# Kernel optimization log

Hardware: AMD Instinct MI355X
Metric: run time of the kernel (lower is better)

Reference implementation:

```python
import jax, jax.numpy as jnp
import numpy as np

NHEAD, HEAD_DIM, UNFOLD = 16, 64, 3
SCALE = np.float32(1.0 / np.sqrt(HEAD_DIM))


def setup_inputs() -> dict:
    key = jax.random.key(0)
    ks = jax.random.split(key, 10)
    B, C, N, L, aL = 1, 256, 64, 256, 2
    D = NHEAD * HEAD_DIM  # 1024
    return {
        "x": jax.random.normal(ks[0], (B, C, N, L, 1), dtype=jnp.float32),
        "ax": jax.random.normal(ks[1], (B, C, N, aL, L), dtype=jnp.float32),
        "wq": jax.random.normal(ks[2], (D, C), dtype=jnp.float32) * 0.02,
        "bq": jax.random.normal(ks[3], (D,), dtype=jnp.float32) * 0.02,
        "wk": jax.random.normal(ks[4], (D, C), dtype=jnp.float32) * 0.02,
        "bk": jax.random.normal(ks[5], (D,), dtype=jnp.float32) * 0.02,
        "wv": jax.random.normal(ks[6], (D, C), dtype=jnp.float32) * 0.02,
        "bv": jax.random.normal(ks[7], (D,), dtype=jnp.float32) * 0.02,
        "wo": jax.random.normal(ks[8], (C, D), dtype=jnp.float32) * 0.02,
        "bo": jax.random.normal(ks[9], (C,), dtype=jnp.float32) * 0.02,
    }


def _proj(x, w, b):
    # x: [B,C,N,L], w: [D,C] -> [B,D,N,L]  (1x1x1 Conv3d == pointwise GEMM)
    return jnp.einsum('bcnl,dc->bdnl', x, w) + b[None, :, None, None]


def reference(x, ax, wq, bq, wk, bk, wv, bv, wo, bo):
    B, C, N, L, _ = x.shape
    x4 = x[..., 0]  # [B,C,N,L]
    q = _proj(x4, wq, bq).reshape(B, NHEAD, HEAD_DIM, N, 1, L)
    k4 = _proj(x4, wk, bk)
    v4 = _proj(x4, wv, bv)

    def unfold(t):
        # F.unfold kernel (3,1), padding (1,0) along N, then the original's
        # .view(B, nhead, head_dim, N, 3, L) applied to [B, C*3, N*L]
        tp = jnp.pad(t, ((0, 0), (0, 0), (1, 1), (0, 0)))
        tw = jnp.stack([tp[:, :, i:i + N, :] for i in range(UNFOLD)], axis=2)  # [B,D,3,N,L]
        return tw.reshape(B, NHEAD, HEAD_DIM, UNFOLD, N, L).reshape(
            B, NHEAD, HEAD_DIM, N, UNFOLD, L)

    k = unfold(k4)
    v = unfold(v4)

    aL = ax.shape[3]
    ak = (jnp.einsum('bcnal,dc->bdnal', ax, wk)
          + bk[None, :, None, None, None]).reshape(B, NHEAD, HEAD_DIM, N, aL, L)
    av = (jnp.einsum('bcnal,dc->bdnal', ax, wv)
          + bv[None, :, None, None, None]).reshape(B, NHEAD, HEAD_DIM, N, aL, L)
    k = jnp.concatenate([k, ak], axis=4)  # [B,H,d,N,3+aL,L]
    v = jnp.concatenate([v, av], axis=4)

    scores = (q * k).sum(2, keepdims=True) * SCALE        # [B,H,1,N,W,L]
    alphas = jax.nn.softmax(scores, axis=4)               # dropout=eval -> identity
    att = (alphas * v).sum(4).reshape(B, NHEAD * HEAD_DIM, N, L)
    out = jnp.einsum('bdnl,cd->bcnl', att, wo) + bo[None, :, None, None]
    return out[..., None]  # [B,nhid,N,L,1]
```

## Files before the change

kernel.cpp:

```cpp
#include <hip/hip_runtime.h>
#include <hip/hip_bf16.h>
#include <stdint.h>

#define N_HEAD 16
#define HDIM 64
#define C_IN 256
#define D_MODEL 1024
#define N_SP 64
#define L_SP 256
#define A_L 2
#define MS (N_SP * L_SP)
#define MA (N_SP * A_L * L_SP)
#define MT (MS + MA)
#define ATT_SCALE 0.125f
#define AUXP 136

typedef __attribute__((ext_vector_type(8))) short bf16x8;
typedef __attribute__((ext_vector_type(4))) float f32x4;
typedef __attribute__((ext_vector_type(8))) unsigned short u16x8;
typedef __attribute__((ext_vector_type(4))) unsigned int u32x4;

static __device__ __forceinline__ __hip_bfloat16 f2bf(float v) { return __float2bfloat16(v); }
static __device__ __forceinline__ unsigned short bfbits(float v) {
    union { __hip_bfloat16 h; unsigned short u; } cv;
    cv.h = __float2bfloat16(v);
    return cv.u;
}
static __device__ __forceinline__ float s2f(short u) {
    union { unsigned int i; float f; } c;
    c.i = ((unsigned int)(unsigned short)u) << 16;
    return c.f;
}

__global__ __launch_bounds__(256) void prep_weights(
    const float* __restrict__ wq, const float* __restrict__ bq,
    const float* __restrict__ wk, const float* __restrict__ bk,
    const float* __restrict__ wv, const float* __restrict__ bv,
    const float* __restrict__ wo,
    __hip_bfloat16* __restrict__ Wqkv, float* __restrict__ BiasQKV,
    __hip_bfloat16* __restrict__ WoB)
{
    int idx = blockIdx.x * 256 + threadIdx.x;
    int row = idx >> 8, col = idx & 255;
    const float* w = (row < D_MODEL) ? wq : (row < 2 * D_MODEL) ? wk : wv;
    Wqkv[idx] = f2bf(w[(size_t)(row & (D_MODEL - 1)) * C_IN + col]);
    if (col == 0) {
        const float* b = (row < D_MODEL) ? bq : (row < 2 * D_MODEL) ? bk : bv;
        BiasQKV[row] = b[row & (D_MODEL - 1)];
    }
    if (idx < C_IN * D_MODEL) WoB[idx] = f2bf(wo[idx]);
}

__global__ __launch_bounds__(256) void transpose_in(
    const float* __restrict__ x, const float* __restrict__ ax,
    __hip_bfloat16* __restrict__ XtAll)
{
    __shared__ float tile[32][33];
    const int tx = threadIdx.x, ty = threadIdx.y;
    const int bx = blockIdx.x;
    const float* src; int M, m0, drow0;
    if (bx < MS / 32) { src = x;  M = MS; m0 = bx * 32;              drow0 = m0; }
    else              { src = ax; M = MA; m0 = (bx - MS / 32) * 32;  drow0 = MS + m0; }
    const int c0 = blockIdx.y * 32;
#pragma unroll
    for (int j = 0; j < 32; j += 8)
        tile[ty + j][tx] = src[(size_t)(c0 + ty + j) * M + m0 + tx];
    __syncthreads();
#pragma unroll
    for (int j = 0; j < 32; j += 8)
        XtAll[(size_t)(drow0 + ty + j) * C_IN + c0 + tx] = f2bf(tile[tx][ty + j]);
}

__global__ __launch_bounds__(256) void gemm_proj(
    const __hip_bfloat16* __restrict__ A,
    const __hip_bfloat16* __restrict__ B,
    __hip_bfloat16* __restrict__ C,
    const float* __restrict__ bias,
    int M, int N, int K)
{
    __shared__ __align__(16) __hip_bfloat16 As[128 * 64];
    __shared__ __align__(16) __hip_bfloat16 Bs[128 * 64];

    const int tid = threadIdx.x;
    const int lane = tid & 63;
    const int w = tid >> 6;
    const int wr = w >> 1, wc = w & 1;
    const int fr = lane & 15, fq = lane >> 4;

    const int nwg = gridDim.x * gridDim.y;
    const int lin = blockIdx.y * gridDim.x + blockIdx.x;
    const int qq = nwg >> 3, rr = nwg & 7;
    const int xcd = lin & 7, ix = lin >> 3;
    const int nlin = (xcd < rr) ? xcd * (qq + 1) + ix
                                : rr * (qq + 1) + (xcd - rr) * qq + ix;
    const int bx = nlin % gridDim.x, by = nlin / gridDim.x;

    const int i0 = by * 128, j0 = bx * 128;
    const int srow = tid >> 3, sch = (tid & 7) << 3;

    f32x4 acc[4][4];
#pragma unroll
    for (int a = 0; a < 4; ++a)
#pragma unroll
        for (int b = 0; b < 4; ++b) acc[a][b] = (f32x4){0.f, 0.f, 0.f, 0.f};

    for (int k0 = 0; k0 < K; k0 += 64) {
        u32x4 ra[4], rb[4];
#pragma unroll
        for (int is = 0; is < 4; ++is) {
            int row = is * 32 + srow;
            ra[is] = *(const u32x4*)(A + (size_t)(i0 + row) * K + k0 + sch);
            rb[is] = *(const u32x4*)(B + (size_t)(j0 + row) * K + k0 + sch);
        }
#pragma unroll
        for (int is = 0; is < 4; ++is) {
            int row = is * 32 + srow;
            *(u32x4*)(As + row * 64 + sch) = ra[is];
            *(u32x4*)(Bs + row * 64 + sch) = rb[is];
        }
        __syncthreads();
#pragma unroll
        for (int kk = 0; kk < 64; kk += 32) {
            bf16x8 af[4], bb[4];
#pragma unroll
            for (int mi = 0; mi < 4; ++mi)
                af[mi] = *(const bf16x8*)(As + (wr * 64 + mi * 16 + fr) * 64 + kk + fq * 8);
#pragma unroll
            for (int ni = 0; ni < 4; ++ni)
                bb[ni] = *(const bf16x8*)(Bs + (wc * 64 + ni * 16 + fr) * 64 + kk + fq * 8);
#pragma unroll
            for (int mi = 0; mi < 4; ++mi)
#pragma unroll
                for (int ni = 0; ni < 4; ++ni)
                    acc[mi][ni] = __builtin_amdgcn_mfma_f32_16x16x32_bf16(
                        af[mi], bb[ni], acc[mi][ni], 0, 0, 0);
        }
        __syncthreads();
    }

#pragma unroll
    for (int mi = 0; mi < 4; ++mi)
#pragma unroll
        for (int r = 0; r < 4; ++r) {
            int row = i0 + wr * 64 + mi * 16 + fq * 4 + r;
#pragma unroll
            for (int ni = 0; ni < 4; ++ni) {
                int col = j0 + wc * 64 + ni * 16 + fr;
                C[(size_t)row * N + col] = f2bf(acc[mi][ni][r] + bias[col]);
            }
        }
}

__global__ __launch_bounds__(256) void attn_fused(
    const __hip_bfloat16* __restrict__ XtAll,
    const __hip_bfloat16* __restrict__ Wqkv,
    const float* __restrict__ BiasQKV,
    __hip_bfloat16* qkv)
{
    __shared__ __align__(16) char ldsraw[36864];
    __hip_bfloat16* As  = (__hip_bfloat16*)ldsraw;
    __hip_bfloat16* Bs  = (__hip_bfloat16*)(ldsraw + 16384);
    __hip_bfloat16* aux = (__hip_bfloat16*)ldsraw;

    const int flat = blockIdx.x;
    const int xcd = flat & 7, idx = flat >> 3;
    const int n  = xcd * 8 + (idx & 7);
    const int h  = (idx >> 3) & 15;
    const int lt = idx >> 7;

    const int tid = threadIdx.x;
    const int lane = tid & 63;
    const int w = tid >> 6;
    const int wr = w >> 1, wc = w & 1;
    const int fr = lane & 15, fq = lane >> 4;
    const int srow = tid >> 3, sch = (tid & 7) << 3;

    f32x4 acc[4][4];
#pragma unroll
    for (int a = 0; a < 4; ++a)
#pragma unroll
        for (int b = 0; b < 4; ++b) acc[a][b] = (f32x4){0.f, 0.f, 0.f, 0.f};

    for (int k0 = 0; k0 < 256; k0 += 64) {
        u32x4 ra[4], rb[4];
#pragma unroll
        for (int is = 0; is < 4; ++is) {
            int r = is * 32 + srow;
            int arow = MS + n * 512 + (r >> 6) * 256 + lt * 64 + (r & 63);
            int brow = 1024 + (r >> 6) * 1024 + h * 64 + (r & 63);
            ra[is] = *(const u32x4*)(XtAll + (size_t)arow * 256 + k0 + sch);
            rb[is] = *(const u32x4*)(Wqkv + (size_t)brow * 256 + k0 + sch);
        }
#pragma unroll
        for (int is = 0; is < 4; ++is) {
            int r = is * 32 + srow;
            *(u32x4*)(As + r * 64 + sch) = ra[is];
            *(u32x4*)(Bs + r * 64 + sch) = rb[is];
        }
        __syncthreads();
#pragma unroll
        for (int kk = 0; kk < 64; kk += 32) {
            bf16x8 af[4], bb[4];
#pragma unroll
            for (int mi = 0; mi < 4; ++mi)
                af[mi] = *(const bf16x8*)(As + (wr * 64 + mi * 16 + fr) * 64 + kk + fq * 8);
#pragma unroll
            for (int ni = 0; ni < 4; ++ni)
                bb[ni] = *(const bf16x8*)(Bs + (wc * 64 + ni * 16 + fr) * 64 + kk + fq * 8);
#pragma unroll
            for (int mi = 0; mi < 4; ++mi)
#pragma unroll
                for (int ni = 0; ni < 4; ++ni)
                    acc[mi][ni] = __builtin_amdgcn_mfma_f32_16x16x32_bf16(
                        af[mi], bb[ni], acc[mi][ni], 0, 0, 0);
        }
        __syncthreads();
    }

    float bcol[4];
#pragma unroll
    for (int ni = 0; ni < 4; ++ni)
        bcol[ni] = BiasQKV[1024 + wc * 1024 + h * 64 + ni * 16 + fr];

#pragma unroll
    for (int mi = 0; mi < 4; ++mi)
#pragma unroll
        for (int r = 0; r < 4; ++r) {
            int row = wr * 64 + mi * 16 + fq * 4 + r;
#pragma unroll
            for (int ni = 0; ni < 4; ++ni) {
                int col = wc * 64 + ni * 16 + fr;
                aux[row * AUXP + col] = f2bf(acc[mi][ni][r] + bcol[ni]);
            }
        }
    __syncthreads();

    const int sub = tid & 3;
    const int ll = tid >> 2;
    const int l = lt * 64 + ll;
    const int m = n * L_SP + l;
    const int ch = sub * 16;

    int src[3]; float val[3];
#pragma unroll
    for (int wd = 0; wd < 3; ++wd) {
        int f = n * 3 + wd;
        int un = f >> 6;
        int nn = (f & 63) + un - 1;
        bool ok = (nn >= 0) && (nn < N_SP);
        src[wd] = ok ? nn : 0;
        val[wd] = ok ? 1.f : 0.f;
    }

    __hip_bfloat16* qp = qkv + (size_t)m * 3072 + h * 64 + ch;
    bf16x8 q0 = *(const bf16x8*)qp, q1 = *(const bf16x8*)(qp + 8);

    bf16x8 kg[3][2], vg[3][2];
#pragma unroll
    for (int wd = 0; wd < 3; ++wd) {
        const __hip_bfloat16* rowp = qkv + (size_t)(src[wd] * L_SP + l) * 3072 + h * 64 + ch;
        kg[wd][0] = *(const bf16x8*)(rowp + 1024);
        kg[wd][1] = *(const bf16x8*)(rowp + 1024 + 8);
        vg[wd][0] = *(const bf16x8*)(rowp + 2048);
        vg[wd][1] = *(const bf16x8*)(rowp + 2048 + 8);
    }
    bf16x8 ka[2][2], va[2][2];
#pragma unroll
    for (int a = 0; a < 2; ++a) {
        const __hip_bfloat16* base = aux + (a * 64 + ll) * AUXP;
        ka[a][0] = *(const bf16x8*)(base + ch);
        ka[a][1] = *(const bf16x8*)(base + ch + 8);
        va[a][0] = *(const bf16x8*)(base + 64 + ch);
        va[a][1] = *(const bf16x8*)(base + 64 + ch + 8);
    }

    float s[5];
#pragma unroll
    for (int i = 0; i < 3; ++i) {
        float d = 0.f;
#pragma unroll
        for (int j = 0; j < 8; ++j)
            d += s2f(q0[j]) * s2f(kg[i][0][j]) + s2f(q1[j]) * s2f(kg[i][1][j]);
        s[i] = d;
    }
#pragma unroll
    for (int a = 0; a < 2; ++a) {
        float d = 0.f;
#pragma unroll
        for (int j = 0; j < 8; ++j)
            d += s2f(q0[j]) * s2f(ka[a][0][j]) + s2f(q1[j]) * s2f(ka[a][1][j]);
        s[3 + a] = d;
    }
#pragma unroll
    for (int i = 0; i < 5; ++i) {
        s[i] += __shfl_xor(s[i], 1);
        s[i] += __shfl_xor(s[i], 2);
        s[i] *= ATT_SCALE;
    }
    s[0] *= val[0]; s[1] *= val[1]; s[2] *= val[2];

    float mx = fmaxf(fmaxf(fmaxf(s[0], s[1]), fmaxf(s[2], s[3])), s[4]);
    float e0 = __expf(s[0] - mx), e1 = __expf(s[1] - mx), e2 = __expf(s[2] - mx);
    float e3 = __expf(s[3] - mx), e4 = __expf(s[4] - mx);
    float inv = 1.f / (e0 + e1 + e2 + e3 + e4);
    float al[5];
    al[0] = e0 * inv * val[0];
    al[1] = e1 * inv * val[1];
    al[2] = e2 * inv * val[2];
    al[3] = e3 * inv;
    al[4] = e4 * inv;

#pragma unroll
    for (int g = 0; g < 2; ++g) {
        u16x8 pack;
#pragma unroll
        for (int j = 0; j < 8; ++j) {
            float o = al[0] * s2f(vg[0][g][j]) + al[1] * s2f(vg[1][g][j])
                    + al[2] * s2f(vg[2][g][j]) + al[3] * s2f(va[0][g][j])
                    + al[4] * s2f(va[1][g][j]);
            pack[j] = bfbits(o);
        }
        *(u16x8*)(qp + g * 8) = pack;
    }
}

__global__ __launch_bounds__(256) void gemm_out(
    const __hip_bfloat16* __restrict__ A,
    const __hip_bfloat16* __restrict__ B,
    float* __restrict__ C,
    const float* __restrict__ bo)
{
    __shared__ __align__(16) __hip_bfloat16 As[128 * 64];
    __shared__ __align__(16) __hip_bfloat16 Bs[128 * 64];

    const int tid = threadIdx.x;
    const int lane = tid & 63;
    const int w = tid >> 6;
    const int wr = w >> 1, wc = w & 1;
    const int fr = lane & 15, fq = lane >> 4;

    const int nwg = gridDim.x * gridDim.y;
    const int lin = blockIdx.y * gridDim.x + blockIdx.x;
    const int qq = nwg >> 3, rr = nwg & 7;
    const int xcd = lin & 7, ix = lin >> 3;
    const int nlin = (xcd < rr) ? xcd * (qq + 1) + ix
                                : rr * (qq + 1) + (xcd - rr) * qq + ix;
    const int bx = nlin % gridDim.x, by = nlin / gridDim.x;

    const int i0 = by * 128, j0 = bx * 128;
    const int srow = tid >> 3, sch = (tid & 7) << 3;

    f32x4 acc[4][4];
#pragma unroll
    for (int a = 0; a < 4; ++a)
#pragma unroll
        for (int b = 0; b < 4; ++b) acc[a][b] = (f32x4){0.f, 0.f, 0.f, 0.f};

    for (int k0 = 0; k0 < 1024; k0 += 64) {
        u32x4 ra[4], rb[4];
#pragma unroll
        for (int is = 0; is < 4; ++is) {
            int row = is * 32 + srow;
            ra[is] = *(const u32x4*)(A + (size_t)(i0 + row) * 1024 + k0 + sch);
            rb[is] = *(const u32x4*)(B + (size_t)(j0 + row) * 3072 + k0 + sch);
        }
#pragma unroll
        for (int is = 0; is < 4; ++is) {
            int row = is * 32 + srow;
            *(u32x4*)(As + row * 64 + sch) = ra[is];
            *(u32x4*)(Bs + row * 64 + sch) = rb[is];
        }
        __syncthreads();
#pragma unroll
        for (int kk = 0; kk < 64; kk += 32) {
            bf16x8 af[4], bb[4];
#pragma unroll
            for (int mi = 0; mi < 4; ++mi)
                af[mi] = *(const bf16x8*)(As + (wr * 64 + mi * 16 + fr) * 64 + kk + fq * 8);
#pragma unroll
            for (int ni = 0; ni < 4; ++ni)
                bb[ni] = *(const bf16x8*)(Bs + (wc * 64 + ni * 16 + fr) * 64 + kk + fq * 8);
#pragma unroll
            for (int mi = 0; mi < 4; ++mi)
#pragma unroll
                for (int ni = 0; ni < 4; ++ni)
                    acc[mi][ni] = __builtin_amdgcn_mfma_f32_16x16x32_bf16(
                        af[mi], bb[ni], acc[mi][ni], 0, 0, 0);
        }
        __syncthreads();
    }

#pragma unroll
    for (int mi = 0; mi < 4; ++mi)
#pragma unroll
        for (int r = 0; r < 4; ++r) {
            int row = i0 + wr * 64 + mi * 16 + fq * 4 + r;
            float bv = bo[row];
#pragma unroll
            for (int ni = 0; ni < 4; ++ni) {
                int col = j0 + wc * 64 + ni * 16 + fr;
                C[(size_t)row * MS + col] = acc[mi][ni][r] + bv;
            }
        }
}

extern "C" void kernel_launch(void* const* d_in, const int* in_sizes, int n_in,
                              void* d_out, int out_size, void* d_ws, size_t ws_size,
                              hipStream_t stream) {
    const float* x  = (const float*)d_in[0];
    const float* ax = (const float*)d_in[1];
    const float* wq = (const float*)d_in[2];
    const float* bq = (const float*)d_in[3];
    const float* wk = (const float*)d_in[4];
    const float* bk = (const float*)d_in[5];
    const float* wv = (const float*)d_in[6];
    const float* bv = (const float*)d_in[7];
    const float* wo = (const float*)d_in[8];
    const float* bo = (const float*)d_in[9];

    auto pad = [](size_t b) { return (b + 255) & ~(size_t)255; };
    char* p = (char*)d_ws;
    auto alloc = [&](size_t bytes) { char* r = p; p += pad(bytes); return r; };

    __hip_bfloat16* Wqkv    = (__hip_bfloat16*)alloc((size_t)3 * D_MODEL * C_IN * 2);
    float*          BiasQKV = (float*)alloc((size_t)3 * D_MODEL * 4);
    __hip_bfloat16* WoB     = (__hip_bfloat16*)alloc((size_t)C_IN * D_MODEL * 2);
    __hip_bfloat16* XtAll   = (__hip_bfloat16*)alloc((size_t)MT * C_IN * 2);
    __hip_bfloat16* qkv_c   = (__hip_bfloat16*)alloc((size_t)MS * 3 * D_MODEL * 2);

    prep_weights<<<dim3(3 * D_MODEL * C_IN / 256), 256, 0, stream>>>(
        wq, bq, wk, bk, wv, bv, wo, Wqkv, BiasQKV, WoB);

    transpose_in<<<dim3(MT / 32, C_IN / 32), dim3(32, 8), 0, stream>>>(x, ax, XtAll);

    gemm_proj<<<dim3(3 * D_MODEL / 128, MS / 128), 256, 0, stream>>>(
        XtAll, Wqkv, qkv_c, BiasQKV, MS, 3 * D_MODEL, C_IN);

    attn_fused<<<dim3(N_SP * N_HEAD * 4), 256, 0, stream>>>(
        XtAll, Wqkv, BiasQKV, qkv_c);

    gemm_out<<<dim3(MS / 128, C_IN / 128), 256, 0, stream>>>(
        WoB, qkv_c, (float*)d_out, bo);
}
```

Baseline: 179.3 us.

## Unfuse aux K/V projection into a separate GEMM and simplify windowed attention

The aux-token K/V projection is moved out of the fused attention kernel and into a standalone call of the generic projection GEMM, which writes a new akv buffer. The attention kernel becomes a pure gather-and-softmax pass with 8 threads per position, each holding 8 channels, and a 3-step shuffle reduction. It now uses twice as many blocks. This removes the small per-block MFMA GEMM and LDS staging from the attention kernel. In exchange, aux K/V makes an extra round trip through global memory (about 64 MB in bf16 written then read), and there is one more kernel launch.

Result: slower. 212.2 us (+18.4%).

```diff
diff --git a/kernel.cpp b/kernel.cpp
--- a/kernel.cpp
+++ b/kernel.cpp
@@ -13,7 +13,6 @@
 #define MA (N_SP * A_L * L_SP)
 #define MT (MS + MA)
 #define ATT_SCALE 0.125f
-#define AUXP 136
 
 typedef __attribute__((ext_vector_type(8))) short bf16x8;
 typedef __attribute__((ext_vector_type(4))) float f32x4;
@@ -151,17 +150,10 @@
         }
 }
 
-__global__ __launch_bounds__(256) void attn_fused(
-    const __hip_bfloat16* __restrict__ XtAll,
-    const __hip_bfloat16* __restrict__ Wqkv,
-    const float* __restrict__ BiasQKV,
-    __hip_bfloat16* qkv)
-{
-    __shared__ __align__(16) char ldsraw[36864];
-    __hip_bfloat16* As  = (__hip_bfloat16*)ldsraw;
-    __hip_bfloat16* Bs  = (__hip_bfloat16*)(ldsraw + 16384);
-    __hip_bfloat16* aux = (__hip_bfloat16*)ldsraw;
-
+__global__ __launch_bounds__(256) void attn_win(
+    __hip_bfloat16* qkv,
+    const __hip_bfloat16* __restrict__ akv)
+{
     const int flat = blockIdx.x;
     const int xcd = flat & 7, idx = flat >> 3;
     const int n  = xcd * 8 + (idx & 7);
@@ -169,77 +161,11 @@
     const int lt = idx >> 7;
 
     const int tid = threadIdx.x;
-    const int lane = tid & 63;
-    const int w = tid >> 6;
-    const int wr = w >> 1, wc = w & 1;
-    const int fr = lane & 15, fq = lane >> 4;
-    const int srow = tid >> 3, sch = (tid & 7) << 3;
-
-    f32x4 acc[4][4];
-#pragma unroll
-    for (int a = 0; a < 4; ++a)
-#pragma unroll
-        for (int b = 0; b < 4; ++b) acc[a][b] = (f32x4){0.f, 0.f, 0.f, 0.f};
-
-    for (int k0 = 0; k0 < 256; k0 += 64) {
-        u32x4 ra[4], rb[4];
-#pragma unroll
-        for (int is = 0; is < 4; ++is) {
-            int r = is * 32 + srow;
-            int arow = MS + n * 512 + (r >> 6) * 256 + lt * 64 + (r & 63);
-            int brow = 1024 + (r >> 6) * 1024 + h * 64 + (r & 63);
-            ra[is] = *(const u32x4*)(XtAll + (size_t)arow * 256 + k0 + sch);
-            rb[is] = *(const u32x4*)(Wqkv + (size_t)brow * 256 + k0 + sch);
-        }
-#pragma unroll
-        for (int is = 0; is < 4; ++is) {
-            int r = is * 32 + srow;
-            *(u32x4*)(As + r * 64 + sch) = ra[is];
-            *(u32x4*)(Bs + r * 64 + sch) = rb[is];
-        }
-        __syncthreads();
-#pragma unroll
-        for (int kk = 0; kk < 64; kk += 32) {
-            bf16x8 af[4], bb[4];
-#pragma unroll
-            for (int mi = 0; mi < 4; ++mi)
-                af[mi] = *(const bf16x8*)(As + (wr * 64 + mi * 16 + fr) * 64 + kk + fq * 8);
-#pragma unroll
-            for (int ni = 0; ni < 4; ++ni)
-                bb[ni] = *(const bf16x8*)(Bs + (wc * 64 + ni * 16 + fr) * 64 + kk + fq * 8);
-#pragma unroll
-            for (int mi = 0; mi < 4; ++mi)
-#pragma unroll
-                for (int ni = 0; ni < 4; ++ni)
-                    acc[mi][ni] = __builtin_amdgcn_mfma_f32_16x16x32_bf16(
-                        af[mi], bb[ni], acc[mi][ni], 0, 0, 0);
-        }
-        __syncthreads();
-    }
-
-    float bcol[4];
-#pragma unroll
-    for (int ni = 0; ni < 4; ++ni)
-        bcol[ni] = BiasQKV[1024 + wc * 1024 + h * 64 + ni * 16 + fr];
-
-#pragma unroll
-    for (int mi = 0; mi < 4; ++mi)
-#pragma unroll
-        for (int r = 0; r < 4; ++r) {
-            int row = wr * 64 + mi * 16 + fq * 4 + r;
-#pragma unroll
-            for (int ni = 0; ni < 4; ++ni) {
-                int col = wc * 64 + ni * 16 + fr;
-                aux[row * AUXP + col] = f2bf(acc[mi][ni][r] + bcol[ni]);
-            }
-        }
-    __syncthreads();
-
-    const int sub = tid & 3;
-    const int ll = tid >> 2;
-    const int l = lt * 64 + ll;
+    const int sub = tid & 7;
+    const int ll = tid >> 3;
+    const int l = lt * 32 + ll;
     const int m = n * L_SP + l;
-    const int ch = sub * 16;
+    const int chb = h * HDIM + sub * 8;
 
     int src[3]; float val[3];
 #pragma unroll
@@ -252,49 +178,35 @@
         val[wd] = ok ? 1.f : 0.f;
     }
 
-    __hip_bfloat16* qp = qkv + (size_t)m * 3072 + h * 64 + ch;
-    bf16x8 q0 = *(const bf16x8*)qp, q1 = *(const bf16x8*)(qp + 8);
-
-    bf16x8 kg[3][2], vg[3][2];
+    __hip_bfloat16* qp = qkv + (size_t)m * 3072 + chb;
+    const bf16x8 q = *(const bf16x8*)qp;
+    bf16x8 kr[5], vr[5];
 #pragma unroll
     for (int wd = 0; wd < 3; ++wd) {
-        const __hip_bfloat16* rowp = qkv + (size_t)(src[wd] * L_SP + l) * 3072 + h * 64 + ch;
-        kg[wd][0] = *(const bf16x8*)(rowp + 1024);
-        kg[wd][1] = *(const bf16x8*)(rowp + 1024 + 8);
-        vg[wd][0] = *(const bf16x8*)(rowp + 2048);
-        vg[wd][1] = *(const bf16x8*)(rowp + 2048 + 8);
-    }
-    bf16x8 ka[2][2], va[2][2];
+        const __hip_bfloat16* rowp = qkv + (size_t)(src[wd] * L_SP + l) * 3072 + chb;
+        kr[wd] = *(const bf16x8*)(rowp + 1024);
+        vr[wd] = *(const bf16x8*)(rowp + 2048);
+    }
 #pragma unroll
     for (int a = 0; a < 2; ++a) {
-        const __hip_bfloat16* base = aux + (a * 64 + ll) * AUXP;
-        ka[a][0] = *(const bf16x8*)(base + ch);
-        ka[a][1] = *(const bf16x8*)(base + ch + 8);
-        va[a][0] = *(const bf16x8*)(base + 64 + ch);
-        va[a][1] = *(const bf16x8*)(base + 64 + ch + 8);
+        const __hip_bfloat16* rowp = akv + (size_t)(n * (A_L * L_SP) + a * L_SP + l) * 2048 + chb;
+        kr[3 + a] = *(const bf16x8*)rowp;
+        vr[3 + a] = *(const bf16x8*)(rowp + 1024);
     }
 
     float s[5];
 #pragma unroll
-    for (int i = 0; i < 3; ++i) {
+    for (int i = 0; i < 5; ++i) {
         float d = 0.f;
 #pragma unroll
-        for (int j = 0; j < 8; ++j)
-            d += s2f(q0[j]) * s2f(kg[i][0][j]) + s2f(q1[j]) * s2f(kg[i][1][j]);
+        for (int j = 0; j < 8; ++j) d += s2f(q[j]) * s2f(kr[i][j]);
         s[i] = d;
-    }
-#pragma unroll
-    for (int a = 0; a < 2; ++a) {
-        float d = 0.f;
-#pragma unroll
-        for (int j = 0; j < 8; ++j)
-            d += s2f(q0[j]) * s2f(ka[a][0][j]) + s2f(q1[j]) * s2f(ka[a][1][j]);
-        s[3 + a] = d;
     }
 #pragma unroll
     for (int i = 0; i < 5; ++i) {
         s[i] += __shfl_xor(s[i], 1);
         s[i] += __shfl_xor(s[i], 2);
+        s[i] += __shfl_xor(s[i], 4);
         s[i] *= ATT_SCALE;
     }
     s[0] *= val[0]; s[1] *= val[1]; s[2] *= val[2];
@@ -310,18 +222,18 @@
     al[3] = e3 * inv;
     al[4] = e4 * inv;
 
-#pragma unroll
-    for (int g = 0; g < 2; ++g) {
-        u16x8 pack;
-#pragma unroll
-        for (int j = 0; j < 8; ++j) {
-            float o = al[0] * s2f(vg[0][g][j]) + al[1] * s2f(vg[1][g][j])
-                    + al[2] * s2f(vg[2][g][j]) + al[3] * s2f(va[0][g][j])
-                    + al[4] * s2f(va[1][g][j]);
-            pack[j] = bfbits(o);
-        }
-        *(u16x8*)(qp + g * 8) = pack;
-    }
+    float o[8];
+#pragma unroll
+    for (int j = 0; j < 8; ++j) o[j] = 0.f;
+#pragma unroll
+    for (int i = 0; i < 5; ++i)
+#pragma unroll
+        for (int j = 0; j < 8; ++j) o[j] += al[i] * s2f(vr[i][j]);
+
+    u16x8 pack;
+#pragma unroll
+    for (int j = 0; j < 8; ++j) pack[j] = bfbits(o[j]);
+    *(u16x8*)qp = pack;
 }
 
 __global__ __launch_bounds__(256) void gemm_out(
@@ -427,6 +339,7 @@
     __hip_bfloat16* WoB     = (__hip_bfloat16*)alloc((size_t)C_IN * D_MODEL * 2);
     __hip_bfloat16* XtAll   = (__hip_bfloat16*)alloc((size_t)MT * C_IN * 2);
     __hip_bfloat16* qkv_c   = (__hip_bfloat16*)alloc((size_t)MS * 3 * D_MODEL * 2);
+    __hip_bfloat16* akv_c   = (__hip_bfloat16*)alloc((size_t)MA * 2 * D_MODEL * 2);
 
     prep_weights<<<dim3(3 * D_MODEL * C_IN / 256), 256, 0, stream>>>(
         wq, bq, wk, bk, wv, bv, wo, Wqkv, BiasQKV, WoB);
@@ -436,8 +349,11 @@
     gemm_proj<<<dim3(3 * D_MODEL / 128, MS / 128), 256, 0, stream>>>(
         XtAll, Wqkv, qkv_c, BiasQKV, MS, 3 * D_MODEL, C_IN);
 
-    attn_fused<<<dim3(N_SP * N_HEAD * 4), 256, 0, stream>>>(
-        XtAll, Wqkv, BiasQKV, qkv_c);
+    gemm_proj<<<dim3(2 * D_MODEL / 128, MA / 128), 256, 0, stream>>>(
+        XtAll + (size_t)MS * C_IN, Wqkv + (size_t)D_MODEL * C_IN, akv_c,
+        BiasQKV + D_MODEL, MA, 2 * D_MODEL, C_IN);
+
+    attn_win<<<dim3(N_SP * N_HEAD * 8), 256, 0, stream>>>(qkv_c, akv_c);
 
     gemm_out<<<dim3(MS / 128, C_IN / 128), 256, 0, stream>>>(
         WoB, qkv_c, (float*)d_out, bo);
```
